# Optimization experiments

Hardware: AMD Instinct MI355X
Metric: run time of the kernel (lower is better)

The kernel has to match this reference:

```python
import jax, jax.numpy as jnp
import numpy as np

B, S, D, H = 2, 2048, 768, 12
HD = D // H


def setup_inputs() -> dict:
    key = jax.random.key(0)
    ks = jax.random.split(key, 8)
    scale = 1.0 / np.sqrt(D)
    inp = {
        "q": jax.random.normal(ks[0], (B, S, D), jnp.float32),
        "k": jax.random.normal(ks[1], (B, S, D), jnp.float32),
        "v": jax.random.normal(ks[2], (B, S, D), jnp.float32),
        # causal mask: 1.0 where attention is disallowed (upper triangle)
        "mask": jnp.triu(jnp.ones((S, S), jnp.float32), k=1)[None, None, :, :],
        "Wq": jax.random.normal(ks[3], (D, D), jnp.float32) * scale,
        "bq": jnp.zeros((D,), jnp.float32),
        "Wk": jax.random.normal(ks[4], (D, D), jnp.float32) * scale,
        "bk": jnp.zeros((D,), jnp.float32),
        "Wv": jax.random.normal(ks[5], (D, D), jnp.float32) * scale,
        "bv": jnp.zeros((D,), jnp.float32),
        "Wo": jax.random.normal(ks[6], (D, D), jnp.float32) * scale,
        "bo": jnp.zeros((D,), jnp.float32),
    }
    return inp


def _split_heads(x):
    # [B, S, D] -> [B, H, S, HD]
    b, s, _ = x.shape
    return x.reshape(b, s, H, HD).transpose(0, 2, 1, 3)


def reference(q, k, v, mask, Wq, bq, Wk, bk, Wv, bv, Wo, bo):
    qh = _split_heads(q @ Wq + bq)
    kh = _split_heads(k @ Wk + bk)
    vh = _split_heads(v @ Wv + bv)
    scale = 1.0 / jnp.sqrt(jnp.asarray(HD, qh.dtype))
    # [B, H, Sq, Sk] — full attention matrix, as in the original
    scores = jnp.einsum("bhqd,bhkd->bhqk", qh, kh) * scale
    scores = scores + mask * -1e9
    attn = jax.nn.softmax(scores, axis=-1)  # dropout is identity at inference
    out = jnp.einsum("bhqk,bhkd->bhqd", attn, vh)
    out = out.transpose(0, 2, 1, 3).reshape(q.shape[0], -1, D)
    return out @ Wo + bo
```

## Files before the change

### kernel.cpp

```cpp
#include <hip/hip_runtime.h>

#define SEQ    2048
#define NB     2
#define DMODEL 768
#define NH     12
#define HDIM   64
#define BS     (NB * SEQ)

typedef __bf16  bf16x8  __attribute__((ext_vector_type(8)));
typedef ushort  ushort8 __attribute__((ext_vector_type(8)));
typedef float   floatx4 __attribute__((ext_vector_type(4)));

#define GLOBAL_AS __attribute__((address_space(1)))
#define LDS_AS    __attribute__((address_space(3)))

union PackU8 { ushort u[8]; uint4 v; };
union PackU4 { ushort u[4]; uint2 v; };

__device__ __forceinline__ ushort f2bf(float x) {
    union { float f; unsigned u; } t; t.f = x;
    unsigned r = t.u + 0x7fffu + ((t.u >> 16) & 1u);
    return (ushort)(r >> 16);
}

__device__ __forceinline__ bf16x8 ld_frag(const ushort* p) {
    return __builtin_bit_cast(bf16x8, *(const ushort8*)p);
}

__global__ void convert_x(const float* __restrict__ q, const float* __restrict__ k,
                          const float* __restrict__ v,
                          ushort* __restrict__ qo, ushort* __restrict__ ko,
                          ushort* __restrict__ vo)
{
    const float* src = blockIdx.z == 0 ? q : blockIdx.z == 1 ? k : v;
    ushort*      dst = blockIdx.z == 0 ? qo : blockIdx.z == 1 ? ko : vo;
    const int i = (blockIdx.x * 256 + threadIdx.x) * 4;
    const float4 f = *(const float4*)(src + i);
    ushort4 o;
    o.x = f2bf(f.x); o.y = f2bf(f.y); o.z = f2bf(f.z); o.w = f2bf(f.w);
    *(ushort4*)(dst + i) = o;
}

__global__ __launch_bounds__(256)
void convert_wT(const float* __restrict__ wq, const float* __restrict__ wk,
                const float* __restrict__ wv, const float* __restrict__ wo,
                ushort* __restrict__ wtcat, ushort* __restrict__ wto)
{
    __shared__ float Tf[64][69];
    const int z = blockIdx.z;
    const float* w = z == 0 ? wq : z == 1 ? wk : z == 2 ? wv : wo;
    ushort*      o = z < 3 ? wtcat + (size_t)z * DMODEL * DMODEL : wto;
    const int k0 = blockIdx.x * 64, n0 = blockIdx.y * 64;
    const int tid = threadIdx.x;
#pragma unroll
    for (int p = 0; p < 4; ++p) {
        const int idx = tid + p * 256;
        const int r = idx >> 4, c = (idx & 15) * 4;
        const float4 f = *(const float4*)&w[(size_t)(k0 + r) * DMODEL + n0 + c];
        Tf[r][c] = f.x; Tf[r][c + 1] = f.y; Tf[r][c + 2] = f.z; Tf[r][c + 3] = f.w;
    }
    __syncthreads();
#pragma unroll
    for (int p = 0; p < 2; ++p) {
        const int idx = tid + p * 256;
        const int n = idx >> 3, kk = (idx & 7) * 8;
        PackU8 pk;
#pragma unroll
        for (int j = 0; j < 8; ++j) pk.u[j] = f2bf(Tf[kk + j][n]);
        *(uint4*)&o[(size_t)(n0 + n) * DMODEL + k0 + kk] = pk.v;
    }
}

__global__ __launch_bounds__(256)
void gemm_qkv(const ushort* __restrict__ xq, const ushort* __restrict__ xk,
              const ushort* __restrict__ xv, const ushort* __restrict__ WT,
              const float* __restrict__ bq, const float* __restrict__ bk,
              const float* __restrict__ bv,
              ushort* __restrict__ oq, ushort* __restrict__ ok,
              ushort* __restrict__ ov)
{
    __shared__ __align__(16) ushort As[128 * 32];
    __shared__ __align__(16) ushort Bs[128 * 32];

    const int z = blockIdx.y / 6;
    const ushort* X = z == 0 ? xq : z == 1 ? xk : xv;

    const int tid  = threadIdx.x;
    const int lane = tid & 63;
    const int w    = tid >> 6;
    const int l15  = lane & 15;
    const int quad = lane >> 4;
    const int wm   = (w >> 1) * 64;
    const int wn   = (w & 1) * 64;
    const int row0 = blockIdx.x * 128;
    const int col0 = blockIdx.y * 128;

    floatx4 acc[4][4];
    const floatx4 fzero = {0.f, 0.f, 0.f, 0.f};
#pragma unroll
    for (int i = 0; i < 4; ++i)
#pragma unroll
        for (int j = 0; j < 4; ++j) acc[i][j] = fzero;

    const int rin = lane >> 2;
    const int gc  = (lane & 3) * 8;

    for (int k0 = 0; k0 < DMODEL; k0 += 32) {
#pragma unroll
        for (int p = 0; p < 2; ++p) {
            const int ch = w * 2 + p;
            const int r  = ch * 16 + rin;
            __builtin_amdgcn_global_load_lds(
                (const GLOBAL_AS uint*)&X[(size_t)(row0 + r) * DMODEL + k0 + gc],
                (LDS_AS uint*)&As[ch * 512], 16, 0, 0);
            __builtin_amdgcn_global_load_lds(
                (const GLOBAL_AS uint*)&WT[(size_t)(col0 + r) * DMODEL + k0 + gc],
                (LDS_AS uint*)&Bs[ch * 512], 16, 0, 0);
        }
        __syncthreads();

        bf16x8 af[4], bfr[4];
#pragma unroll
        for (int t = 0; t < 4; ++t) {
            af[t]  = ld_frag(&As[(wm + t * 16 + l15) * 32 + quad * 8]);
            bfr[t] = ld_frag(&Bs[(wn + t * 16 + l15) * 32 + quad * 8]);
        }
#pragma unroll
        for (int ti = 0; ti < 4; ++ti)
#pragma unroll
            for (int tj = 0; tj < 4; ++tj)
                acc[ti][tj] = __builtin_amdgcn_mfma_f32_16x16x32_bf16(
                    af[ti], bfr[tj], acc[ti][tj], 0, 0, 0);
        __syncthreads();
    }

    const int c0 = (blockIdx.y % 6) * 128;
    const float*  bias = z == 0 ? bq : z == 1 ? bk : bv;
    ushort*       out  = z == 0 ? oq : z == 1 ? ok : ov;
#pragma unroll
    for (int tj = 0; tj < 4; ++tj) {
        const int c_l = c0 + wn + tj * 16 + l15;
        const float bb = bias[c_l];
        const int h  = c_l >> 6;
        const int dd = c_l & 63;
#pragma unroll
        for (int ti = 0; ti < 4; ++ti) {
#pragma unroll
            for (int ri = 0; ri < 4; ++ri) {
                const int r_g = row0 + wm + ti * 16 + quad * 4 + ri;
                const int b   = r_g >> 11;
                const int s   = r_g & (SEQ - 1);
                out[(((size_t)(b * NH + h) * SEQ + s) << 6) + dd] =
                    f2bf(acc[ti][tj][ri] + bb);
            }
        }
    }
}

__global__ __launch_bounds__(256)
void gemm_out(const ushort* __restrict__ X, const ushort* __restrict__ WT,
              const float* __restrict__ bias, float* __restrict__ fo)
{
    __shared__ __align__(16) ushort As[64][40];
    __shared__ __align__(16) ushort Bs[128][40];

    const int tid  = threadIdx.x;
    const int lane = tid & 63;
    const int wv   = tid >> 6;
    const int wm   = (wv >> 1) * 32;
    const int wn   = (wv & 1) * 64;
    const int l15  = lane & 15;
    const int quad = lane >> 4;
    const int row0 = blockIdx.x * 64;
    const int col0 = blockIdx.y * 128;

    floatx4 acc[2][4];
    const floatx4 fzero = {0.f, 0.f, 0.f, 0.f};
#pragma unroll
    for (int i = 0; i < 2; ++i)
#pragma unroll
        for (int j = 0; j < 4; ++j) acc[i][j] = fzero;

    const int sr = tid >> 2;
    const int sc = (tid & 3) * 8;

    for (int k0 = 0; k0 < DMODEL; k0 += 32) {
        *(uint4*)&As[sr][sc] = *(const uint4*)&X[(size_t)(row0 + sr) * DMODEL + k0 + sc];
#pragma unroll
        for (int p = 0; p < 2; ++p) {
            const int r = sr + p * 64;
            *(uint4*)&Bs[r][sc] = *(const uint4*)&WT[(size_t)(col0 + r) * DMODEL + k0 + sc];
        }
        __syncthreads();

        bf16x8 af[2], bfr[4];
#pragma unroll
        for (int t = 0; t < 2; ++t)
            af[t] = ld_frag(&As[wm + t * 16 + l15][quad * 8]);
#pragma unroll
        for (int t = 0; t < 4; ++t)
            bfr[t] = ld_frag(&Bs[wn + t * 16 + l15][quad * 8]);
#pragma unroll
        for (int ti = 0; ti < 2; ++ti)
#pragma unroll
            for (int tj = 0; tj < 4; ++tj)
                acc[ti][tj] = __builtin_amdgcn_mfma_f32_16x16x32_bf16(
                    af[ti], bfr[tj], acc[ti][tj], 0, 0, 0);
        __syncthreads();
    }

#pragma unroll
    for (int tj = 0; tj < 4; ++tj) {
        const int c_g = col0 + wn + tj * 16 + l15;
        const float bb = bias[c_g];
#pragma unroll
        for (int ti = 0; ti < 2; ++ti)
#pragma unroll
            for (int ri = 0; ri < 4; ++ri) {
                const int r_g = row0 + wm + ti * 16 + quad * 4 + ri;
                fo[(size_t)r_g * DMODEL + c_g] = acc[ti][tj][ri] + bb;
            }
    }
}

__global__ void transpose_v(const ushort* __restrict__ vh, ushort* __restrict__ vt)
{
    __shared__ __align__(16) ushort T[64][72];
    const int bh = blockIdx.y;
    const int s0 = blockIdx.x * 64;
    const ushort* src = vh + (size_t)bh * SEQ * HDIM;
    ushort*       dst = vt + (size_t)bh * HDIM * SEQ;

#pragma unroll
    for (int p = 0; p < 2; ++p) {
        const int idx = threadIdx.x + p * 256;
        const int r = idx >> 3, c = (idx & 7) * 8;
        *(uint4*)&T[r][c] = *(const uint4*)&src[(size_t)(s0 + r) * HDIM + c];
    }
    __syncthreads();
#pragma unroll
    for (int p = 0; p < 2; ++p) {
        const int idx = threadIdx.x + p * 256;
        const int d = idx >> 3, c = (idx & 7) * 8;
        PackU8 pk;
#pragma unroll
        for (int j = 0; j < 8; ++j) pk.u[j] = T[c + j][d];
        *(uint4*)&dst[(size_t)d * SEQ + s0 + c] = pk.v;
    }
}

#define APAD 88

__device__ __forceinline__ void attn_epilogue(ushort* __restrict__ ctx, int b, int h,
                                              int qtile, int wv, int quad, int l15,
                                              const floatx4* O, float l)
{
    const float inv = 1.f / l;
    float ib[4];
#pragma unroll
    for (int ri = 0; ri < 4; ++ri) ib[ri] = __shfl(inv, quad * 4 + ri);
#pragma unroll
    for (int dj = 0; dj < 4; ++dj)
#pragma unroll
        for (int ri = 0; ri < 4; ++ri) {
            const int row = qtile * 32 + wv * 16 + quad * 4 + ri;
            ctx[((size_t)b * SEQ + row) * DMODEL + h * HDIM + dj * 16 + l15] =
                f2bf(O[dj][ri] * ib[ri]);
        }
}

__global__ __launch_bounds__(128)
void attn_mfma(const ushort* __restrict__ qh, const ushort* __restrict__ kh,
               const ushort* __restrict__ vt, ushort* __restrict__ ctx)
{
    __shared__ __align__(16) ushort Ks[2][64][APAD];
    __shared__ __align__(16) ushort Vs[2][64][APAD];
    __shared__ __align__(16) ushort Ps[32][APAD];

    const int tid  = threadIdx.x;
    const int lane = tid & 63;
    const int wv   = tid >> 6;
    const int l15  = lane & 15;
    const int quad = lane >> 4;
    const int id  = blockIdx.x;
    const int xcd = id & 7;
    const int jj  = id >> 3;
    const int g   = jj >> 5;
    const int x   = jj & 31;
    const int bh  = xcd + 8 * g;
    const int b   = bh / NH, h = bh - b * NH;
    const int qA  = x, qB = 63 - x;
    const int nkA = (qA >> 1) + 1;
    const size_t base = (size_t)bh * SEQ * HDIM;

    const float SCL = 0.125f * 1.44269504f;

    bf16x8 qfA[2], qfB[2];
#pragma unroll
    for (int ks = 0; ks < 2; ++ks) {
        qfA[ks] = ld_frag(&qh[base + (size_t)(qA * 32 + wv * 16 + l15) * HDIM + ks * 32 + quad * 8]);
        qfB[ks] = ld_frag(&qh[base + (size_t)(qB * 32 + wv * 16 + l15) * HDIM + ks * 32 + quad * 8]);
    }

    const int sr = tid >> 3;
    const int sc = (tid & 7) * 8;

    uint4 kreg[4], vreg[4];
#pragma unroll
    for (int p = 0; p < 4; ++p) {
        const int r = sr + p * 16;
        kreg[p] = *(const uint4*)&kh[base + (size_t)r * HDIM + sc];
        vreg[p] = *(const uint4*)&vt[base + (size_t)r * SEQ + sc];
    }
#pragma unroll
    for (int p = 0; p < 4; ++p) {
        const int r = sr + p * 16;
        *(uint4*)&Ks[0][r][sc] = kreg[p];
        *(uint4*)&Vs[0][r][sc] = vreg[p];
    }

    float l = 0.f;
    floatx4 O[4];
    const floatx4 fzero = {0.f, 0.f, 0.f, 0.f};
#pragma unroll
    for (int dj = 0; dj < 4; ++dj) O[dj] = fzero;

    const int rowA = qA * 32 + wv * 16 + l15;
    const int rowB = qB * 32 + wv * 16 + l15;

    for (int t = 0; t <= 32; ++t) {
        __syncthreads();
        const int buf = t & 1;

        if (t < 32) {
            const int kn  = (t + 1 < nkA) ? (t + 1) : (t + 1 - nkA);
            const int c0n = kn * 64;
#pragma unroll
            for (int p = 0; p < 4; ++p) {
                const int r = sr + p * 16;
                kreg[p] = *(const uint4*)&kh[base + (size_t)(c0n + r) * HDIM + sc];
                vreg[p] = *(const uint4*)&vt[base + (size_t)r * SEQ + c0n + sc];
            }
        }

        const bool isA   = (t < nkA);
        const int  kt    = isA ? t : t - nkA;
        const int  c0    = kt * 64;
        const bool diag  = (t == nkA - 1) || (t == 32);
        const int  row_g = isA ? rowA : rowB;

        floatx4 S[4];
#pragma unroll
        for (int nj = 0; nj < 4; ++nj) {
            S[nj] = fzero;
#pragma unroll
            for (int ks = 0; ks < 2; ++ks) {
                const bf16x8 kf = ld_frag(&Ks[buf][nj * 16 + l15][ks * 32 + quad * 8]);
                const bf16x8 qf = isA ? qfA[ks] : qfB[ks];
                S[nj] = __builtin_amdgcn_mfma_f32_16x16x32_bf16(kf, qf, S[nj], 0, 0, 0);
            }
        }

        float rs = 0.f;
#pragma unroll
        for (int nj = 0; nj < 4; ++nj) {
            PackU4 pk;
#pragma unroll
            for (int ri = 0; ri < 4; ++ri) {
                float p = __builtin_amdgcn_exp2f(S[nj][ri] * SCL);
                if (diag && (c0 + nj * 16 + quad * 4 + ri > row_g)) p = 0.f;
                rs += p;
                union { float f; unsigned u; } tb; tb.f = p;
                pk.u[ri] = (ushort)(tb.u >> 16);
            }
            *(uint2*)&Ps[wv * 16 + l15][nj * 16 + quad * 4] = pk.v;
        }
        rs += __shfl_xor(rs, 16);
        rs += __shfl_xor(rs, 32);
        l += rs;

        bf16x8 pf[2];
#pragma unroll
        for (int ks = 0; ks < 2; ++ks)
            pf[ks] = ld_frag(&Ps[wv * 16 + l15][ks * 32 + quad * 8]);
#pragma unroll
        for (int dj = 0; dj < 4; ++dj)
#pragma unroll
            for (int ks = 0; ks < 2; ++ks) {
                const bf16x8 vfr = ld_frag(&Vs[buf][dj * 16 + l15][ks * 32 + quad * 8]);
                O[dj] = __builtin_amdgcn_mfma_f32_16x16x32_bf16(pf[ks], vfr, O[dj], 0, 0, 0);
            }

        if (t == nkA - 1) {
            attn_epilogue(ctx, b, h, qA, wv, quad, l15, O, l);
            l = 0.f;
#pragma unroll
            for (int dj = 0; dj < 4; ++dj) O[dj] = fzero;
        }

        if (t < 32) {
#pragma unroll
            for (int p = 0; p < 4; ++p) {
                const int r = sr + p * 16;
                *(uint4*)&Ks[buf ^ 1][r][sc] = kreg[p];
                *(uint4*)&Vs[buf ^ 1][r][sc] = vreg[p];
            }
        }
    }

    attn_epilogue(ctx, b, h, qB, wv, quad, l15, O, l);
}

extern "C" void kernel_launch(void* const* d_in, const int* in_sizes, int n_in,
                              void* d_out, int out_size, void* d_ws, size_t ws_size,
                              hipStream_t stream)
{
    const float* q  = (const float*)d_in[0];
    const float* k  = (const float*)d_in[1];
    const float* v  = (const float*)d_in[2];
    const float* Wq = (const float*)d_in[4];
    const float* bq = (const float*)d_in[5];
    const float* Wk = (const float*)d_in[6];
    const float* bk = (const float*)d_in[7];
    const float* Wv = (const float*)d_in[8];
    const float* bv = (const float*)d_in[9];
    const float* Wo = (const float*)d_in[10];
    const float* bo = (const float*)d_in[11];
    float* out = (float*)d_out;

    char* ws = (char*)d_ws;
    const size_t ACT = (size_t)BS * DMODEL * 2;
    ushort* qx    = (ushort*)(ws);
    ushort* kx    = (ushort*)(ws + ACT);
    ushort* vx    = (ushort*)(ws + 2 * ACT);
    ushort* qhp   = (ushort*)(ws + 3 * ACT);
    ushort* khp   = (ushort*)(ws + 4 * ACT);
    ushort* vhp   = (ushort*)(ws + 5 * ACT);
    ushort* wtcat = (ushort*)(ws + 6 * ACT);
    ushort* wto   = wtcat + (size_t)3 * DMODEL * DMODEL;
    ushort* vhT   = vx;
    ushort* ctx   = qx;

    convert_x<<<dim3(BS * DMODEL / 1024, 1, 3), 256, 0, stream>>>(q, k, v, qx, kx, vx);
    convert_wT<<<dim3(12, 12, 4), 256, 0, stream>>>(Wq, Wk, Wv, Wo, wtcat, wto);
    gemm_qkv<<<dim3(BS / 128, 18), 256, 0, stream>>>(
        qx, kx, vx, wtcat, bq, bk, bv, qhp, khp, vhp);
    transpose_v<<<dim3(SEQ / 64, NB * NH), 256, 0, stream>>>(vhp, vhT);
    attn_mfma<<<dim3(768), 128, 0, stream>>>(qhp, khp, vhT, ctx);
    gemm_out<<<dim3(BS / 64, DMODEL / 128), 256, 0, stream>>>(ctx, wto, bo, out);
}
```

Before: 207.7 us.

## Fuse V transpose into QKV GEMM epilogue and restructure attention scheduling

The QKV projection epilogue now writes V directly in transposed [b,h,d,s] layout, which removes the separate transpose_v kernel launch and its extra memory round trip. The attention kernel drops the paired-tile load balancing (one block handling q-tiles x and 63-x) in favour of one q-tile per block, with 1536 blocks ordered longest-first. It also replaces padded LDS rows with an XOR swizzle and uses a perm-based bf16 pack. The risk is that single-tile blocks are less evenly balanced, and the transposed V stores from the GEMM are narrow scattered 8-byte writes.

```diff
diff --git a/kernel.cpp b/kernel.cpp
--- a/kernel.cpp
+++ b/kernel.cpp
@@ -15,12 +15,16 @@
 #define LDS_AS    __attribute__((address_space(3)))
 
 union PackU8 { ushort u[8]; uint4 v; };
-union PackU4 { ushort u[4]; uint2 v; };
 
 __device__ __forceinline__ ushort f2bf(float x) {
     union { float f; unsigned u; } t; t.f = x;
     unsigned r = t.u + 0x7fffu + ((t.u >> 16) & 1u);
     return (ushort)(r >> 16);
+}
+
+__device__ __forceinline__ unsigned bfpack(float hi, float lo) {
+    union { float f; unsigned u; } a, b; a.f = hi; b.f = lo;
+    return __builtin_amdgcn_perm(a.u, b.u, 0x07060302u);
 }
 
 __device__ __forceinline__ bf16x8 ld_frag(const ushort* p) {
@@ -77,7 +81,7 @@
               const float* __restrict__ bq, const float* __restrict__ bk,
               const float* __restrict__ bv,
               ushort* __restrict__ oq, ushort* __restrict__ ok,
-              ushort* __restrict__ ov)
+              ushort* __restrict__ ovT)
 {
     __shared__ __align__(16) ushort As[128 * 32];
     __shared__ __align__(16) ushort Bs[128 * 32];
@@ -136,7 +140,8 @@
 
     const int c0 = (blockIdx.y % 6) * 128;
     const float*  bias = z == 0 ? bq : z == 1 ? bk : bv;
-    ushort*       out  = z == 0 ? oq : z == 1 ? ok : ov;
+    ushort*       out  = z == 0 ? oq : ok;
+
 #pragma unroll
     for (int tj = 0; tj < 4; ++tj) {
         const int c_l = c0 + wn + tj * 16 + l15;
@@ -145,13 +150,19 @@
         const int dd = c_l & 63;
 #pragma unroll
         for (int ti = 0; ti < 4; ++ti) {
-#pragma unroll
-            for (int ri = 0; ri < 4; ++ri) {
-                const int r_g = row0 + wm + ti * 16 + quad * 4 + ri;
-                const int b   = r_g >> 11;
-                const int s   = r_g & (SEQ - 1);
-                out[(((size_t)(b * NH + h) * SEQ + s) << 6) + dd] =
-                    f2bf(acc[ti][tj][ri] + bb);
+            const int r0 = row0 + wm + ti * 16 + quad * 4;
+            const int b  = r0 >> 11;
+            const int s0 = r0 & (SEQ - 1);
+            if (z == 2) {
+                uint2 pk;
+                pk.x = ((unsigned)f2bf(acc[ti][tj][1] + bb) << 16) | f2bf(acc[ti][tj][0] + bb);
+                pk.y = ((unsigned)f2bf(acc[ti][tj][3] + bb) << 16) | f2bf(acc[ti][tj][2] + bb);
+                *(uint2*)&ovT[(((size_t)(b * NH + h) * HDIM + dd) << 11) + s0] = pk;
+            } else {
+#pragma unroll
+                for (int ri = 0; ri < 4; ++ri)
+                    out[(((size_t)(b * NH + h) * SEQ + s0 + ri) << 6) + dd] =
+                        f2bf(acc[ti][tj][ri] + bb);
             }
         }
     }
@@ -223,100 +234,54 @@
     }
 }
 
-__global__ void transpose_v(const ushort* __restrict__ vh, ushort* __restrict__ vt)
-{
-    __shared__ __align__(16) ushort T[64][72];
-    const int bh = blockIdx.y;
-    const int s0 = blockIdx.x * 64;
-    const ushort* src = vh + (size_t)bh * SEQ * HDIM;
-    ushort*       dst = vt + (size_t)bh * HDIM * SEQ;
-
-#pragma unroll
-    for (int p = 0; p < 2; ++p) {
-        const int idx = threadIdx.x + p * 256;
-        const int r = idx >> 3, c = (idx & 7) * 8;
-        *(uint4*)&T[r][c] = *(const uint4*)&src[(size_t)(s0 + r) * HDIM + c];
-    }
-    __syncthreads();
-#pragma unroll
-    for (int p = 0; p < 2; ++p) {
-        const int idx = threadIdx.x + p * 256;
-        const int d = idx >> 3, c = (idx & 7) * 8;
-        PackU8 pk;
-#pragma unroll
-        for (int j = 0; j < 8; ++j) pk.u[j] = T[c + j][d];
-        *(uint4*)&dst[(size_t)d * SEQ + s0 + c] = pk.v;
-    }
-}
-
-#define APAD 88
-
-__device__ __forceinline__ void attn_epilogue(ushort* __restrict__ ctx, int b, int h,
-                                              int qtile, int wv, int quad, int l15,
-                                              const floatx4* O, float l)
-{
-    const float inv = 1.f / l;
-    float ib[4];
-#pragma unroll
-    for (int ri = 0; ri < 4; ++ri) ib[ri] = __shfl(inv, quad * 4 + ri);
-#pragma unroll
-    for (int dj = 0; dj < 4; ++dj)
-#pragma unroll
-        for (int ri = 0; ri < 4; ++ri) {
-            const int row = qtile * 32 + wv * 16 + quad * 4 + ri;
-            ctx[((size_t)b * SEQ + row) * DMODEL + h * HDIM + dj * 16 + l15] =
-                f2bf(O[dj][ri] * ib[ri]);
-        }
-}
-
 __global__ __launch_bounds__(128)
 void attn_mfma(const ushort* __restrict__ qh, const ushort* __restrict__ kh,
                const ushort* __restrict__ vt, ushort* __restrict__ ctx)
 {
-    __shared__ __align__(16) ushort Ks[2][64][APAD];
-    __shared__ __align__(16) ushort Vs[2][64][APAD];
-    __shared__ __align__(16) ushort Ps[32][APAD];
+    __shared__ __align__(16) ushort Ks[2][64 * 64];
+    __shared__ __align__(16) ushort Vs[2][64 * 64];
+    __shared__ __align__(16) ushort Ps[32 * 64];
 
     const int tid  = threadIdx.x;
     const int lane = tid & 63;
-    const int wv   = tid >> 6;
+    const int w    = tid >> 6;
     const int l15  = lane & 15;
     const int quad = lane >> 4;
-    const int id  = blockIdx.x;
-    const int xcd = id & 7;
-    const int jj  = id >> 3;
-    const int g   = jj >> 5;
-    const int x   = jj & 31;
-    const int bh  = xcd + 8 * g;
-    const int b   = bh / NH, h = bh - b * NH;
-    const int qA  = x, qB = 63 - x;
-    const int nkA = (qA >> 1) + 1;
+    const int id   = blockIdx.x;
+    const int xcd  = id & 7;
+    const int rr   = id >> 3;
+    const int g    = rr >> 6;
+    const int qt   = 63 - (rr & 63);
+    const int bh   = xcd + 8 * g;
+    const int b    = bh / NH, h = bh - b * NH;
+    const int nk   = (qt >> 1) + 1;
     const size_t base = (size_t)bh * SEQ * HDIM;
 
     const float SCL = 0.125f * 1.44269504f;
-
-    bf16x8 qfA[2], qfB[2];
-#pragma unroll
-    for (int ks = 0; ks < 2; ++ks) {
-        qfA[ks] = ld_frag(&qh[base + (size_t)(qA * 32 + wv * 16 + l15) * HDIM + ks * 32 + quad * 8]);
-        qfB[ks] = ld_frag(&qh[base + (size_t)(qB * 32 + wv * 16 + l15) * HDIM + ks * 32 + quad * 8]);
-    }
-
-    const int sr = tid >> 3;
-    const int sc = (tid & 7) * 8;
+    const int   swz = l15 & 7;
+
+    bf16x8 qf[2];
+#pragma unroll
+    for (int ks = 0; ks < 2; ++ks)
+        qf[ks] = ld_frag(&qh[base + (size_t)(qt * 32 + w * 16 + l15) * HDIM
+                              + ks * 32 + quad * 8]);
+
+    const int sr  = tid >> 3;
+    const int sch = tid & 7;
+    const int scw = ((sch ^ (sr & 7)) * 8);
 
     uint4 kreg[4], vreg[4];
 #pragma unroll
     for (int p = 0; p < 4; ++p) {
         const int r = sr + p * 16;
-        kreg[p] = *(const uint4*)&kh[base + (size_t)r * HDIM + sc];
-        vreg[p] = *(const uint4*)&vt[base + (size_t)r * SEQ + sc];
+        kreg[p] = *(const uint4*)&kh[base + (size_t)r * HDIM + sch * 8];
+        vreg[p] = *(const uint4*)&vt[base + (size_t)r * SEQ + sch * 8];
     }
 #pragma unroll
     for (int p = 0; p < 4; ++p) {
         const int r = sr + p * 16;
-        *(uint4*)&Ks[0][r][sc] = kreg[p];
-        *(uint4*)&Vs[0][r][sc] = vreg[p];
+        *(uint4*)&Ks[0][r * 64 + scw] = kreg[p];
+        *(uint4*)&Vs[0][r * 64 + scw] = vreg[p];
     }
 
     float l = 0.f;
@@ -325,29 +290,24 @@
 #pragma unroll
     for (int dj = 0; dj < 4; ++dj) O[dj] = fzero;
 
-    const int rowA = qA * 32 + wv * 16 + l15;
-    const int rowB = qB * 32 + wv * 16 + l15;
-
-    for (int t = 0; t <= 32; ++t) {
+    const int qrow = qt * 32 + w * 16 + l15;
+
+    for (int t = 0; t < nk; ++t) {
         __syncthreads();
         const int buf = t & 1;
 
-        if (t < 32) {
-            const int kn  = (t + 1 < nkA) ? (t + 1) : (t + 1 - nkA);
-            const int c0n = kn * 64;
+        if (t + 1 < nk) {
+            const int c0n = (t + 1) * 64;
 #pragma unroll
             for (int p = 0; p < 4; ++p) {
                 const int r = sr + p * 16;
-                kreg[p] = *(const uint4*)&kh[base + (size_t)(c0n + r) * HDIM + sc];
-                vreg[p] = *(const uint4*)&vt[base + (size_t)r * SEQ + c0n + sc];
-            }
-        }
-
-        const bool isA   = (t < nkA);
-        const int  kt    = isA ? t : t - nkA;
-        const int  c0    = kt * 64;
-        const bool diag  = (t == nkA - 1) || (t == 32);
-        const int  row_g = isA ? rowA : rowB;
+                kreg[p] = *(const uint4*)&kh[base + (size_t)(c0n + r) * HDIM + sch * 8];
+                vreg[p] = *(const uint4*)&vt[base + (size_t)r * SEQ + c0n + sch * 8];
+            }
+        }
+
+        const int  c0   = t * 64;
+        const bool diag = (t == nk - 1);
 
         floatx4 S[4];
 #pragma unroll
@@ -355,25 +315,30 @@
             S[nj] = fzero;
 #pragma unroll
             for (int ks = 0; ks < 2; ++ks) {
-                const bf16x8 kf = ld_frag(&Ks[buf][nj * 16 + l15][ks * 32 + quad * 8]);
-                const bf16x8 qf = isA ? qfA[ks] : qfB[ks];
-                S[nj] = __builtin_amdgcn_mfma_f32_16x16x32_bf16(kf, qf, S[nj], 0, 0, 0);
+                const bf16x8 kf = ld_frag(
+                    &Ks[buf][(nj * 16 + l15) * 64 + ((ks * 4 + quad) ^ swz) * 8]);
+                S[nj] = __builtin_amdgcn_mfma_f32_16x16x32_bf16(kf, qf[ks], S[nj], 0, 0, 0);
             }
         }
 
         float rs = 0.f;
 #pragma unroll
         for (int nj = 0; nj < 4; ++nj) {
-            PackU4 pk;
-#pragma unroll
-            for (int ri = 0; ri < 4; ++ri) {
-                float p = __builtin_amdgcn_exp2f(S[nj][ri] * SCL);
-                if (diag && (c0 + nj * 16 + quad * 4 + ri > row_g)) p = 0.f;
-                rs += p;
-                union { float f; unsigned u; } tb; tb.f = p;
-                pk.u[ri] = (ushort)(tb.u >> 16);
-            }
-            *(uint2*)&Ps[wv * 16 + l15][nj * 16 + quad * 4] = pk.v;
+            float p[4];
+#pragma unroll
+            for (int ri = 0; ri < 4; ++ri)
+                p[ri] = __builtin_amdgcn_exp2f(S[nj][ri] * SCL);
+            if (diag) {
+#pragma unroll
+                for (int ri = 0; ri < 4; ++ri)
+                    if (c0 + nj * 16 + quad * 4 + ri > qrow) p[ri] = 0.f;
+            }
+            rs += (p[0] + p[1]) + (p[2] + p[3]);
+            uint2 pk;
+            pk.x = bfpack(p[1], p[0]);
+            pk.y = bfpack(p[3], p[2]);
+            const int cw = ((2 * nj + (quad >> 1)) ^ swz);
+            *(uint2*)&Ps[(w * 16 + l15) * 64 + cw * 8 + (quad & 1) * 4] = pk;
         }
         rs += __shfl_xor(rs, 16);
         rs += __shfl_xor(rs, 32);
@@ -382,33 +347,39 @@
         bf16x8 pf[2];
 #pragma unroll
         for (int ks = 0; ks < 2; ++ks)
-            pf[ks] = ld_frag(&Ps[wv * 16 + l15][ks * 32 + quad * 8]);
+            pf[ks] = ld_frag(&Ps[(w * 16 + l15) * 64 + ((ks * 4 + quad) ^ swz) * 8]);
 #pragma unroll
         for (int dj = 0; dj < 4; ++dj)
 #pragma unroll
             for (int ks = 0; ks < 2; ++ks) {
-                const bf16x8 vfr = ld_frag(&Vs[buf][dj * 16 + l15][ks * 32 + quad * 8]);
+                const bf16x8 vfr = ld_frag(
+                    &Vs[buf][(dj * 16 + l15) * 64 + ((ks * 4 + quad) ^ swz) * 8]);
                 O[dj] = __builtin_amdgcn_mfma_f32_16x16x32_bf16(pf[ks], vfr, O[dj], 0, 0, 0);
             }
 
-        if (t == nkA - 1) {
-            attn_epilogue(ctx, b, h, qA, wv, quad, l15, O, l);
-            l = 0.f;
-#pragma unroll
-            for (int dj = 0; dj < 4; ++dj) O[dj] = fzero;
-        }
-
-        if (t < 32) {
+        if (t + 1 < nk) {
 #pragma unroll
             for (int p = 0; p < 4; ++p) {
                 const int r = sr + p * 16;
-                *(uint4*)&Ks[buf ^ 1][r][sc] = kreg[p];
-                *(uint4*)&Vs[buf ^ 1][r][sc] = vreg[p];
-            }
-        }
-    }
-
-    attn_epilogue(ctx, b, h, qB, wv, quad, l15, O, l);
+                *(uint4*)&Ks[buf ^ 1][r * 64 + scw] = kreg[p];
+                *(uint4*)&Vs[buf ^ 1][r * 64 + scw] = vreg[p];
+            }
+        }
+    }
+
+    const float inv = 1.f / l;
+    float ib[4];
+#pragma unroll
+    for (int ri = 0; ri < 4; ++ri) ib[ri] = __shfl(inv, quad * 4 + ri);
+#pragma unroll
+    for (int dj = 0; dj < 4; ++dj) {
+        const int col = h * HDIM + dj * 16 + l15;
+#pragma unroll
+        for (int ri = 0; ri < 4; ++ri) {
+            const int row = qt * 32 + w * 16 + quad * 4 + ri;
+            ctx[((size_t)b * SEQ + row) * DMODEL + col] = f2bf(O[dj][ri] * ib[ri]);
+        }
+    }
 }
 
 extern "C" void kernel_launch(void* const* d_in, const int* in_sizes, int n_in,
@@ -435,17 +406,15 @@
     ushort* vx    = (ushort*)(ws + 2 * ACT);
     ushort* qhp   = (ushort*)(ws + 3 * ACT);
     ushort* khp   = (ushort*)(ws + 4 * ACT);
-    ushort* vhp   = (ushort*)(ws + 5 * ACT);
+    ushort* vhT   = (ushort*)(ws + 5 * ACT);
     ushort* wtcat = (ushort*)(ws + 6 * ACT);
     ushort* wto   = wtcat + (size_t)3 * DMODEL * DMODEL;
-    ushort* vhT   = vx;
     ushort* ctx   = qx;
 
     convert_x<<<dim3(BS * DMODEL / 1024, 1, 3), 256, 0, stream>>>(q, k, v, qx, kx, vx);
     convert_wT<<<dim3(12, 12, 4), 256, 0, stream>>>(Wq, Wk, Wv, Wo, wtcat, wto);
     gemm_qkv<<<dim3(BS / 128, 18), 256, 0, stream>>>(
-        qx, kx, vx, wtcat, bq, bk, bv, qhp, khp, vhp);
-    transpose_v<<<dim3(SEQ / 64, NB * NH), 256, 0, stream>>>(vhp, vhT);
-    attn_mfma<<<dim3(768), 128, 0, stream>>>(qhp, khp, vhT, ctx);
+        qx, kx, vx, wtcat, bq, bk, bv, qhp, khp, vhT);
+    attn_mfma<<<dim3(1536), 128, 0, stream>>>(qhp, khp, vhT, ctx);
     gemm_out<<<dim3(BS / 64, DMODEL / 128), 256, 0, stream>>>(ctx, wto, bo, out);
 }
```

Result: slower. 270.8 us (+30.4%).

## Double attention query tile to 64 rows per block, halve grid

Applied to the files above, without the earlier changes.

Each attention block now processes 64-row query tiles, with each wave handling two 16-row subtiles, instead of 32-row tiles. Every K/V tile staged in LDS is reused for twice as many query rows, which halves the K/V global traffic and the number of blocks to 384. In exchange, register pressure rises from the doubled O, S and Q fragments, and the smaller grid lowers occupancy and parallelism on the GPU. The causal pairing of tiles (x with 31-x) keeps the work per block balanced.

```diff
diff --git a/kernel.cpp b/kernel.cpp
--- a/kernel.cpp
+++ b/kernel.cpp
@@ -252,7 +252,7 @@
 #define APAD 88
 
 __device__ __forceinline__ void attn_epilogue(ushort* __restrict__ ctx, int b, int h,
-                                              int qtile, int wv, int quad, int l15,
+                                              int row0, int quad, int l15,
                                               const floatx4* O, float l)
 {
     const float inv = 1.f / l;
@@ -263,7 +263,7 @@
     for (int dj = 0; dj < 4; ++dj)
 #pragma unroll
         for (int ri = 0; ri < 4; ++ri) {
-            const int row = qtile * 32 + wv * 16 + quad * 4 + ri;
+            const int row = row0 + quad * 4 + ri;
             ctx[((size_t)b * SEQ + row) * DMODEL + h * HDIM + dj * 16 + l15] =
                 f2bf(O[dj][ri] * ib[ri]);
         }
@@ -275,7 +275,7 @@
 {
     __shared__ __align__(16) ushort Ks[2][64][APAD];
     __shared__ __align__(16) ushort Vs[2][64][APAD];
-    __shared__ __align__(16) ushort Ps[32][APAD];
+    __shared__ __align__(16) ushort Ps[64][APAD];
 
     const int tid  = threadIdx.x;
     const int lane = tid & 63;
@@ -285,22 +285,26 @@
     const int id  = blockIdx.x;
     const int xcd = id & 7;
     const int jj  = id >> 3;
-    const int g   = jj >> 5;
-    const int x   = jj & 31;
+    const int g   = jj >> 4;
+    const int x   = jj & 15;
     const int bh  = xcd + 8 * g;
     const int b   = bh / NH, h = bh - b * NH;
-    const int qA  = x, qB = 63 - x;
-    const int nkA = (qA >> 1) + 1;
+    const int qA  = x, qB = 31 - x;
+    const int nkA = qA + 1;
     const size_t base = (size_t)bh * SEQ * HDIM;
 
     const float SCL = 0.125f * 1.44269504f;
 
-    bf16x8 qfA[2], qfB[2];
-#pragma unroll
-    for (int ks = 0; ks < 2; ++ks) {
-        qfA[ks] = ld_frag(&qh[base + (size_t)(qA * 32 + wv * 16 + l15) * HDIM + ks * 32 + quad * 8]);
-        qfB[ks] = ld_frag(&qh[base + (size_t)(qB * 32 + wv * 16 + l15) * HDIM + ks * 32 + quad * 8]);
-    }
+    bf16x8 qfA[2][2], qfB[2][2];
+#pragma unroll
+    for (int u = 0; u < 2; ++u)
+#pragma unroll
+        for (int ks = 0; ks < 2; ++ks) {
+            qfA[u][ks] = ld_frag(&qh[base + (size_t)(qA * 64 + wv * 32 + u * 16 + l15) * HDIM
+                                      + ks * 32 + quad * 8]);
+            qfB[u][ks] = ld_frag(&qh[base + (size_t)(qB * 64 + wv * 32 + u * 16 + l15) * HDIM
+                                      + ks * 32 + quad * 8]);
+        }
 
     const int sr = tid >> 3;
     const int sc = (tid & 7) * 8;
@@ -319,14 +323,16 @@
         *(uint4*)&Vs[0][r][sc] = vreg[p];
     }
 
-    float l = 0.f;
-    floatx4 O[4];
+    float l[2] = {0.f, 0.f};
+    floatx4 O[2][4];
     const floatx4 fzero = {0.f, 0.f, 0.f, 0.f};
 #pragma unroll
-    for (int dj = 0; dj < 4; ++dj) O[dj] = fzero;
-
-    const int rowA = qA * 32 + wv * 16 + l15;
-    const int rowB = qB * 32 + wv * 16 + l15;
+    for (int u = 0; u < 2; ++u)
+#pragma unroll
+        for (int dj = 0; dj < 4; ++dj) O[u][dj] = fzero;
+
+    const int rowA0 = qA * 64 + wv * 32;
+    const int rowB0 = qB * 64 + wv * 32;
 
     for (int t = 0; t <= 32; ++t) {
         __syncthreads();
@@ -343,59 +349,75 @@
             }
         }
 
-        const bool isA   = (t < nkA);
-        const int  kt    = isA ? t : t - nkA;
-        const int  c0    = kt * 64;
-        const bool diag  = (t == nkA - 1) || (t == 32);
-        const int  row_g = isA ? rowA : rowB;
-
-        floatx4 S[4];
+        const bool isA  = (t < nkA);
+        const int  kt   = isA ? t : t - nkA;
+        const int  c0   = kt * 64;
+        const bool diag = (t == nkA - 1) || (t == 32);
+        const int  r0   = isA ? rowA0 : rowB0;
+
+        floatx4 S[2][4];
 #pragma unroll
         for (int nj = 0; nj < 4; ++nj) {
-            S[nj] = fzero;
+#pragma unroll
+            for (int u = 0; u < 2; ++u) S[u][nj] = fzero;
 #pragma unroll
             for (int ks = 0; ks < 2; ++ks) {
                 const bf16x8 kf = ld_frag(&Ks[buf][nj * 16 + l15][ks * 32 + quad * 8]);
-                const bf16x8 qf = isA ? qfA[ks] : qfB[ks];
-                S[nj] = __builtin_amdgcn_mfma_f32_16x16x32_bf16(kf, qf, S[nj], 0, 0, 0);
-            }
-        }
-
-        float rs = 0.f;
-#pragma unroll
-        for (int nj = 0; nj < 4; ++nj) {
-            PackU4 pk;
-#pragma unroll
-            for (int ri = 0; ri < 4; ++ri) {
-                float p = __builtin_amdgcn_exp2f(S[nj][ri] * SCL);
-                if (diag && (c0 + nj * 16 + quad * 4 + ri > row_g)) p = 0.f;
-                rs += p;
-                union { float f; unsigned u; } tb; tb.f = p;
-                pk.u[ri] = (ushort)(tb.u >> 16);
-            }
-            *(uint2*)&Ps[wv * 16 + l15][nj * 16 + quad * 4] = pk.v;
-        }
-        rs += __shfl_xor(rs, 16);
-        rs += __shfl_xor(rs, 32);
-        l += rs;
-
-        bf16x8 pf[2];
-#pragma unroll
-        for (int ks = 0; ks < 2; ++ks)
-            pf[ks] = ld_frag(&Ps[wv * 16 + l15][ks * 32 + quad * 8]);
+#pragma unroll
+                for (int u = 0; u < 2; ++u) {
+                    const bf16x8 qf = isA ? qfA[u][ks] : qfB[u][ks];
+                    S[u][nj] = __builtin_amdgcn_mfma_f32_16x16x32_bf16(kf, qf, S[u][nj], 0, 0, 0);
+                }
+            }
+        }
+
+#pragma unroll
+        for (int u = 0; u < 2; ++u) {
+            const int row_g = r0 + u * 16 + l15;
+            float rs = 0.f;
+#pragma unroll
+            for (int nj = 0; nj < 4; ++nj) {
+                PackU4 pk;
+#pragma unroll
+                for (int ri = 0; ri < 4; ++ri) {
+                    float p = __builtin_amdgcn_exp2f(S[u][nj][ri] * SCL);
+                    if (diag && (c0 + nj * 16 + quad * 4 + ri > row_g)) p = 0.f;
+                    rs += p;
+                    union { float f; unsigned uu; } tb; tb.f = p;
+                    pk.u[ri] = (ushort)(tb.uu >> 16);
+                }
+                *(uint2*)&Ps[wv * 32 + u * 16 + l15][nj * 16 + quad * 4] = pk.v;
+            }
+            rs += __shfl_xor(rs, 16);
+            rs += __shfl_xor(rs, 32);
+            l[u] += rs;
+        }
+
+        bf16x8 pf[2][2];
+#pragma unroll
+        for (int u = 0; u < 2; ++u)
+#pragma unroll
+            for (int ks = 0; ks < 2; ++ks)
+                pf[u][ks] = ld_frag(&Ps[wv * 32 + u * 16 + l15][ks * 32 + quad * 8]);
 #pragma unroll
         for (int dj = 0; dj < 4; ++dj)
 #pragma unroll
             for (int ks = 0; ks < 2; ++ks) {
                 const bf16x8 vfr = ld_frag(&Vs[buf][dj * 16 + l15][ks * 32 + quad * 8]);
-                O[dj] = __builtin_amdgcn_mfma_f32_16x16x32_bf16(pf[ks], vfr, O[dj], 0, 0, 0);
+#pragma unroll
+                for (int u = 0; u < 2; ++u)
+                    O[u][dj] = __builtin_amdgcn_mfma_f32_16x16x32_bf16(
+                        pf[u][ks], vfr, O[u][dj], 0, 0, 0);
             }
 
         if (t == nkA - 1) {
-            attn_epilogue(ctx, b, h, qA, wv, quad, l15, O, l);
-            l = 0.f;
-#pragma unroll
-            for (int dj = 0; dj < 4; ++dj) O[dj] = fzero;
+#pragma unroll
+            for (int u = 0; u < 2; ++u) {
+                attn_epilogue(ctx, b, h, rowA0 + u * 16, quad, l15, O[u], l[u]);
+                l[u] = 0.f;
+#pragma unroll
+                for (int dj = 0; dj < 4; ++dj) O[u][dj] = fzero;
+            }
         }
 
         if (t < 32) {
@@ -408,7 +430,9 @@
         }
     }
 
-    attn_epilogue(ctx, b, h, qB, wv, quad, l15, O, l);
+#pragma unroll
+    for (int u = 0; u < 2; ++u)
+        attn_epilogue(ctx, b, h, rowB0 + u * 16, quad, l15, O[u], l[u]);
 }
 
 extern "C" void kernel_launch(void* const* d_in, const int* in_sizes, int n_in,
@@ -446,6 +470,6 @@
     gemm_qkv<<<dim3(BS / 128, 18), 256, 0, stream>>>(
         qx, kx, vx, wtcat, bq, bk, bv, qhp, khp, vhp);
     transpose_v<<<dim3(SEQ / 64, NB * NH), 256, 0, stream>>>(vhp, vhT);
-    attn_mfma<<<dim3(768), 128, 0, stream>>>(qhp, khp, vhT, ctx);
+    attn_mfma<<<dim3(384), 128, 0, stream>>>(qhp, khp, vhT, ctx);
     gemm_out<<<dim3(BS / 64, DMODEL / 128), 256, 0, stream>>>(ctx, wto, bo, out);
 }
```

Result: slower. 218.5 us (+5.2%).
